# Kernel tuning notes

Measured on AMD Instinct MI355X. Metric: run time of the kernel, lower is better.

Reference implementation:

```python
import jax, jax.numpy as jnp
import numpy as np

B, T, C, H = 2, 2048, 1024, 16
D = C // H  # head dim = 64


def setup_inputs() -> dict:
    key = jax.random.key(0)
    k1, k2, k3 = jax.random.split(key, 3)
    s = 1.0 / np.sqrt(C)
    return {
        "x": jax.random.normal(k1, (B, T, C), dtype=jnp.float32),
        "w_qkv": jax.random.normal(k2, (C, 3 * C), dtype=jnp.float32) * s,
        "b_qkv": jnp.zeros((3 * C,), dtype=jnp.float32),
        "w_proj": jax.random.normal(k3, (C, C), dtype=jnp.float32) * s,
        "b_proj": jnp.zeros((C,), dtype=jnp.float32),
    }


def reference(x, w_qkv, b_qkv, w_proj, b_proj):
    Bx, Tx, Cx = x.shape
    qkv = x @ w_qkv + b_qkv                      # [B,T,3C]
    q, k, v = jnp.split(qkv, 3, axis=-1)         # each [B,T,C]
    # split heads -> [B,H,T,D]
    q = q.reshape(Bx, Tx, H, D).transpose(0, 2, 1, 3)
    k = k.reshape(Bx, Tx, H, D).transpose(0, 2, 1, 3)
    v = v.reshape(Bx, Tx, H, D).transpose(0, 2, 1, 3)
    att = jnp.einsum("bhqd,bhkd->bhqk", q, k) * (1.0 / np.sqrt(D))
    causal = jnp.tril(jnp.ones((Tx, Tx), dtype=bool))
    att = jnp.where(causal, att, -jnp.inf)
    att = jax.nn.softmax(att, axis=-1)
    y = jnp.einsum("bhqk,bhkd->bhqd", att, v)    # [B,H,T,D]
    y = y.transpose(0, 2, 1, 3).reshape(Bx, Tx, Cx)
    return y @ w_proj + b_proj
```

## Files before the change

kernel.cpp:

```cpp
#include <hip/hip_runtime.h>


typedef __attribute__((ext_vector_type(8))) __bf16 bf16x8;
typedef __attribute__((ext_vector_type(4))) __bf16 bf16x4;
typedef __attribute__((ext_vector_type(4))) float f32x4;
typedef __attribute__((ext_vector_type(8))) unsigned short u16x8;
typedef __attribute__((ext_vector_type(4))) unsigned short u16x4;

#define GAS __attribute__((address_space(1)))
#define LAS __attribute__((address_space(3)))

__device__ __forceinline__ unsigned short f2b(float f) {
  unsigned int u = __float_as_uint(f);
  unsigned int r = 0x7FFFu + ((u >> 16) & 1u);
  return (unsigned short)((u + r) >> 16);
}
__device__ __forceinline__ float b2f(unsigned short u) {
  return __uint_as_float((unsigned int)u << 16);
}


__global__ void cvt_f32_to_bf16(const float* __restrict__ src,
                                unsigned short* __restrict__ dst, int n4) {
  int i = blockIdx.x * blockDim.x + threadIdx.x;
  if (i < n4) {
    float4 v = ((const float4*)src)[i];
    u16x4 o = { f2b(v.x), f2b(v.y), f2b(v.z), f2b(v.w) };
    *(u16x4*)(dst + (size_t)i * 4) = o;
  }
}

__global__ void transpose_f32_to_bf16(const float* __restrict__ src,
                                      unsigned short* __restrict__ dst,
                                      int K, int N) {
  __shared__ float tile[32][33];
  int n0 = blockIdx.x * 32, k0 = blockIdx.y * 32;
  int tx = threadIdx.x, ty = threadIdx.y;
#pragma unroll
  for (int i = 0; i < 32; i += 8)
    tile[ty + i][tx] = src[(size_t)(k0 + ty + i) * N + n0 + tx];
  __syncthreads();
#pragma unroll
  for (int i = 0; i < 32; i += 8)
    dst[(size_t)(n0 + ty + i) * K + k0 + tx] = f2b(tile[tx][ty + i]);
}


template <int MODE>
__global__ void __launch_bounds__(256, 3) gemm_bt(
    const unsigned short* __restrict__ A, const unsigned short* __restrict__ Bt,
    const float* __restrict__ bias,
    unsigned short* __restrict__ Oq, unsigned short* __restrict__ Ok,
    unsigned short* __restrict__ Ov, float* __restrict__ Of,
    int M, int N, int K) {
  __shared__ unsigned short smem[3 * 128 * 64];
  unsigned short* As = smem;
  unsigned short* Bs = smem + 3 * 128 * 32;

  const int tid = threadIdx.x;
  const int lane = tid & 63;
  const int wid = tid >> 6;
  const int wr = wid >> 1, wc = wid & 1;
  const int lr = lane & 15, lg = lane >> 4;
  const int m0 = blockIdx.x * 128;
  const int n0 = blockIdx.y * 128;

  f32x4 acc[4][4];
#pragma unroll
  for (int mi = 0; mi < 4; mi++)
#pragma unroll
    for (int ni = 0; ni < 4; ni++) acc[mi][ni] = (f32x4){0.f, 0.f, 0.f, 0.f};

  auto stage = [&](int t, int buf) {
    const int k0 = t * 32;
    unsigned short* Ad = As + buf * (128 * 32);
    unsigned short* Bd = Bs + buf * (128 * 32);
#pragma unroll
    for (int it = 0; it < 2; ++it) {
      const int chunk_u = it * 256 + (tid & ~63);
      const int chunk = chunk_u + lane;
      const int row = chunk >> 2;
      const int col = ((chunk & 3) ^ ((row >> 1) & 3)) * 8;
      __builtin_amdgcn_global_load_lds(
          (GAS unsigned int*)(A + (size_t)(m0 + row) * K + k0 + col),
          (LAS unsigned int*)(Ad + chunk_u * 8), 16, 0, 0);
      __builtin_amdgcn_global_load_lds(
          (GAS unsigned int*)(Bt + (size_t)(n0 + row) * K + k0 + col),
          (LAS unsigned int*)(Bd + chunk_u * 8), 16, 0, 0);
    }
  };

  const int kt = K >> 5;
  const int rsw = (lg ^ ((lr >> 1) & 3)) * 8;

  stage(0, 0);
  stage(1, 1);

  int cur = 0;
  for (int t = 0; t < kt; ++t) {
    __builtin_amdgcn_s_barrier();
    if (t + 2 < kt) {
      int pb = cur + 2; if (pb >= 3) pb -= 3;
      stage(t + 2, pb);
      asm volatile("s_waitcnt vmcnt(8)" ::: "memory");
    } else if (t + 1 < kt) {
      asm volatile("s_waitcnt vmcnt(4)" ::: "memory");
    } else {
      asm volatile("s_waitcnt vmcnt(0)" ::: "memory");
    }
    __builtin_amdgcn_s_barrier();

    const unsigned short* Ab = As + cur * (128 * 32);
    const unsigned short* Bb = Bs + cur * (128 * 32);

    bf16x8 af[4], bfr[4];
#pragma unroll
    for (int mi = 0; mi < 4; mi++)
      af[mi] = *(const bf16x8*)(Ab + (wr * 64 + mi * 16 + lr) * 32 + rsw);
#pragma unroll
    for (int ni = 0; ni < 4; ni++)
      bfr[ni] = *(const bf16x8*)(Bb + (wc * 64 + ni * 16 + lr) * 32 + rsw);
    __builtin_amdgcn_s_setprio(1);
#pragma unroll
    for (int mi = 0; mi < 4; mi++)
#pragma unroll
      for (int ni = 0; ni < 4; ni++)
        acc[mi][ni] = __builtin_amdgcn_mfma_f32_16x16x32_bf16(
            af[mi], bfr[ni], acc[mi][ni], 0, 0, 0);
    __builtin_amdgcn_s_setprio(0);

    cur += 1; if (cur >= 3) cur -= 3;
  }

  const float SCLQ = 0.125f * 1.44269504088896340736f;

  if constexpr (MODE == 1) {
#pragma unroll
    for (int mi = 0; mi < 4; mi++) {
#pragma unroll
      for (int ni = 0; ni < 4; ni++) {
        const int nn = n0 + wc * 64 + ni * 16 + lr;
        const float bv = bias[nn];
#pragma unroll
        for (int r = 0; r < 4; r++) {
          const int mm = m0 + wr * 64 + mi * 16 + lg * 4 + r;
          Of[(size_t)mm * N + nn] = acc[mi][ni][r] + bv;
        }
      }
    }
  } else {
    unsigned short* L = smem;
    const int which = n0 >> 10;
    const float sc = (which == 0) ? SCLQ : 1.0f;
    __syncthreads();
#pragma unroll
    for (int mi = 0; mi < 4; mi++) {
#pragma unroll
      for (int ni = 0; ni < 4; ni++) {
        const int nn_l = wc * 64 + ni * 16 + lr;
        const float bv = bias[n0 + nn_l];
#pragma unroll
        for (int r = 0; r < 4; r++) {
          const int mm_l = wr * 64 + mi * 16 + lg * 4 + r;
          const unsigned short v = f2b((acc[mi][ni][r] + bv) * sc);
          if (which == 2) L[nn_l * 136 + mm_l] = v;
          else            L[mm_l * 136 + nn_l] = v;
        }
      }
    }
    __syncthreads();
    const int b = m0 >> 11;
    const int t0 = m0 & 2047;
    const int h0 = (n0 & 1023) >> 6;
    if (which == 2) {
      const int row = tid >> 1;
      const int hsub = row >> 6, d = row & 63;
      const int tt0 = (tid & 1) * 64;
      const unsigned short* src = L + row * 136 + tt0;
      unsigned short* dst = Ov +
          ((size_t)((b * 16 + h0 + hsub) * 64 + d)) * 2048 + t0 + tt0;
#pragma unroll
      for (int j = 0; j < 8; j++)
        *(u16x8*)(dst + j * 8) = *(const u16x8*)(src + j * 8);
    } else {
      const int mm_l = tid & 127;
      const int hsub = tid >> 7;
      const unsigned short* src = L + mm_l * 136 + hsub * 64;
      unsigned short* base = (which == 0) ? Oq : Ok;
      unsigned short* dst = base +
          ((size_t)(b * 16 + h0 + hsub) * 2048 + t0 + mm_l) * 64;
#pragma unroll
      for (int j = 0; j < 8; j++)
        *(u16x8*)(dst + j * 8) = *(const u16x8*)(src + j * 8);
    }
  }
}


__global__ void __launch_bounds__(256, 3) attn_kernel(
    const unsigned short* __restrict__ Qh, const unsigned short* __restrict__ Kh,
    const unsigned short* __restrict__ Vh, unsigned short* __restrict__ yatt,
    unsigned short* __restrict__ Opart, float* __restrict__ Mp,
    float* __restrict__ Lp) {
  __shared__ unsigned short KsL[2 * 64 * 64];
  __shared__ unsigned short VsL[2 * 64 * 64];
  __shared__ unsigned short Pl[4 * 32 * 72];

  const int tid = threadIdx.x;
  const int lane = tid & 63;
  const int w = tid >> 6;
  const int lr = lane & 15, lg = lane >> 4;

  const int cls = blockIdx.x >> 5;
  const int bh = blockIdx.x & 31;
  const int hh = bh & 15;
  const int bb = bh >> 4;

  const unsigned long long QA = 0x8899AABBCCDDEEFFull;
  const unsigned long long QB = 0x0000014425566377ull;
  const unsigned long long KK = 0x00A4912444444444ull;
  const int qt = (cls < 16) ? (int)((QA >> (4 * cls)) & 15)
                            : (int)((QB >> (4 * (cls - 16))) & 15);
  const int kind = (int)((KK >> (2 * cls)) & 3);
  const int t0 = (kind == 1) ? (qt + 1) : 0;
  const int t1 = (kind == 0) ? (qt + 1) : (2 * qt + 2);

  const size_t head_base = ((size_t)(bb * 16 + hh)) * 2048 * 64;
  const unsigned short* Qg = Qh + head_base;
  const unsigned short* Kg = Kh + head_base;
  const unsigned short* Vg = Vh + head_base;

  const int q0 = qt * 128 + w * 32;
  const int diagw = 2 * qt + (w >> 1);

  bf16x8 aqA0 = *(const bf16x8*)(Qg + (size_t)(q0 + lr) * 64 + lg * 8);
  bf16x8 aqA1 = *(const bf16x8*)(Qg + (size_t)(q0 + lr) * 64 + 32 + lg * 8);
  bf16x8 aqB0 = *(const bf16x8*)(Qg + (size_t)(q0 + 16 + lr) * 64 + lg * 8);
  bf16x8 aqB1 = *(const bf16x8*)(Qg + (size_t)(q0 + 16 + lr) * 64 + 32 + lg * 8);

  float mA = -__builtin_inff(), mB = -__builtin_inff();
  float lA = 0.f, lB = 0.f;
  f32x4 oA[4], oB[4];
#pragma unroll
  for (int dj = 0; dj < 4; dj++) {
    oA[dj] = (f32x4){0.f, 0.f, 0.f, 0.f};
    oB[dj] = (f32x4){0.f, 0.f, 0.f, 0.f};
  }

  auto stage = [&](int kv0, int buf) {
    unsigned short* Kd = KsL + buf * (64 * 64);
    unsigned short* Vd = VsL + buf * (64 * 64);
#pragma unroll
    for (int it = 0; it < 2; ++it) {
      const int chunk_u = it * 256 + (tid & ~63);
      const int chunk = chunk_u + lane;
      const int row = chunk >> 3;
      const int col = ((chunk & 7) ^ (row & 7)) << 3;
      __builtin_amdgcn_global_load_lds(
          (GAS unsigned int*)(Kg + (size_t)(kv0 + row) * 64 + col),
          (LAS unsigned int*)(Kd + chunk_u * 8), 16, 0, 0);
      __builtin_amdgcn_global_load_lds(
          (GAS unsigned int*)(Vg + (size_t)row * 2048 + kv0 + col),
          (LAS unsigned int*)(Vd + chunk_u * 8), 16, 0, 0);
    }
  };

  __bf16* Pw = (__bf16*)(Pl + w * 32 * 72);
  const int swr = (lr & 7) << 3;
  const int pswz = (lr & 3) << 4;

  stage(t0 * 64, t0 & 1);

  for (int i = t0; i < t1; ++i) {
    const int cur = i & 1;
    __builtin_amdgcn_s_barrier();
    if (i + 1 < t1) {
      stage((i + 1) * 64, cur ^ 1);
      asm volatile("s_waitcnt vmcnt(4)" ::: "memory");
    } else {
      asm volatile("s_waitcnt vmcnt(0)" ::: "memory");
    }
    __builtin_amdgcn_s_barrier();

    if (i <= diagw) {
      const int kv0 = i * 64;
      const unsigned short* Kb = KsL + cur * (64 * 64);
      const unsigned short* Vb = VsL + cur * (64 * 64);

      f32x4 sA[4], sB[4];
      __builtin_amdgcn_s_setprio(1);
#pragma unroll
      for (int nj = 0; nj < 4; nj++) {
        const unsigned short* krow = Kb + (nj * 16 + lr) * 64;
        bf16x8 kb0 = *(const bf16x8*)(krow + ((lg * 8) ^ swr));
        bf16x8 kb1 = *(const bf16x8*)(krow + ((32 + lg * 8) ^ swr));
        f32x4 zA = (f32x4){0.f, 0.f, 0.f, 0.f};
        f32x4 zB = (f32x4){0.f, 0.f, 0.f, 0.f};
        zA = __builtin_amdgcn_mfma_f32_16x16x32_bf16(kb0, aqA0, zA, 0, 0, 0);
        zA = __builtin_amdgcn_mfma_f32_16x16x32_bf16(kb1, aqA1, zA, 0, 0, 0);
        zB = __builtin_amdgcn_mfma_f32_16x16x32_bf16(kb0, aqB0, zB, 0, 0, 0);
        zB = __builtin_amdgcn_mfma_f32_16x16x32_bf16(kb1, aqB1, zB, 0, 0, 0);
        sA[nj] = zA;
        sB[nj] = zB;
      }
      __builtin_amdgcn_s_setprio(0);

      if (i == diagw) {
        const int qrA = q0 + lr, qrB = q0 + 16 + lr;
#pragma unroll
        for (int nj = 0; nj < 4; nj++) {
#pragma unroll
          for (int r = 0; r < 4; r++) {
            const int key = kv0 + nj * 16 + lg * 4 + r;
            if (key > qrA) sA[nj][r] = -__builtin_inff();
            if (key > qrB) sB[nj][r] = -__builtin_inff();
          }
        }
      }

      float pmA = sA[0][0], pmB = sB[0][0];
#pragma unroll
      for (int nj = 0; nj < 4; nj++)
#pragma unroll
        for (int r = 0; r < 4; r++) {
          pmA = fmaxf(pmA, sA[nj][r]);
          pmB = fmaxf(pmB, sB[nj][r]);
        }

      const bool okl = (pmA <= mA + 8.f) & (pmB <= mB + 8.f);
      if (!__all(okl)) {
        pmA = fmaxf(pmA, __shfl_xor(pmA, 16));
        pmA = fmaxf(pmA, __shfl_xor(pmA, 32));
        pmB = fmaxf(pmB, __shfl_xor(pmB, 16));
        pmB = fmaxf(pmB, __shfl_xor(pmB, 32));
        const float mnA = fmaxf(mA, pmA), mnB = fmaxf(mB, pmB);
        const float scA = exp2f(mA - mnA), scB = exp2f(mB - mnB);
        mA = mnA; mB = mnB;
        lA *= scA; lB *= scB;
#pragma unroll
        for (int r = 0; r < 4; r++) {
          const float cA = __shfl(scA, lg * 4 + r);
          const float cB = __shfl(scB, lg * 4 + r);
#pragma unroll
          for (int dj = 0; dj < 4; dj++) {
            oA[dj][r] *= cA;
            oB[dj][r] *= cB;
          }
        }
      }

#pragma unroll
      for (int nj = 0; nj < 4; nj++) {
        const float a0 = exp2f(sA[nj][0] - mA), a1 = exp2f(sA[nj][1] - mA);
        const float a2 = exp2f(sA[nj][2] - mA), a3 = exp2f(sA[nj][3] - mA);
        lA += (a0 + a1) + (a2 + a3);
        bf16x4 pkA = {(__bf16)a0, (__bf16)a1, (__bf16)a2, (__bf16)a3};
        *(bf16x4*)(Pw + lr * 72 + ((nj * 16 + lg * 4) ^ pswz)) = pkA;
        const float b0 = exp2f(sB[nj][0] - mB), b1 = exp2f(sB[nj][1] - mB);
        const float b2 = exp2f(sB[nj][2] - mB), b3 = exp2f(sB[nj][3] - mB);
        lB += (b0 + b1) + (b2 + b3);
        bf16x4 pkB = {(__bf16)b0, (__bf16)b1, (__bf16)b2, (__bf16)b3};
        *(bf16x4*)(Pw + (16 + lr) * 72 + ((nj * 16 + lg * 4) ^ pswz)) = pkB;
      }

      bf16x8 paA0 = *(const bf16x8*)(Pw + lr * 72 + ((lg * 8) ^ pswz));
      bf16x8 paA1 = *(const bf16x8*)(Pw + lr * 72 + ((32 + lg * 8) ^ pswz));
      bf16x8 paB0 = *(const bf16x8*)(Pw + (16 + lr) * 72 + ((lg * 8) ^ pswz));
      bf16x8 paB1 = *(const bf16x8*)(Pw + (16 + lr) * 72 + ((32 + lg * 8) ^ pswz));

      __builtin_amdgcn_s_setprio(1);
#pragma unroll
      for (int dj = 0; dj < 4; dj++) {
        const unsigned short* vrow = Vb + (dj * 16 + lr) * 64;
        bf16x8 vb0 = *(const bf16x8*)(vrow + ((lg * 8) ^ swr));
        bf16x8 vb1 = *(const bf16x8*)(vrow + ((32 + lg * 8) ^ swr));
        oA[dj] = __builtin_amdgcn_mfma_f32_16x16x32_bf16(paA0, vb0, oA[dj], 0, 0, 0);
        oA[dj] = __builtin_amdgcn_mfma_f32_16x16x32_bf16(paA1, vb1, oA[dj], 0, 0, 0);
        oB[dj] = __builtin_amdgcn_mfma_f32_16x16x32_bf16(paB0, vb0, oB[dj], 0, 0, 0);
        oB[dj] = __builtin_amdgcn_mfma_f32_16x16x32_bf16(paB1, vb1, oB[dj], 0, 0, 0);
      }
      __builtin_amdgcn_s_setprio(0);
    }
  }

  lA += __shfl_xor(lA, 16); lA += __shfl_xor(lA, 32);
  lB += __shfl_xor(lB, 16); lB += __shfl_xor(lB, 32);

  if (kind == 2) {
    __bf16* yb = (__bf16*)yatt;
#pragma unroll
    for (int r = 0; r < 4; r++) {
      const float invA = 1.0f / __shfl(lA, lg * 4 + r);
      const float invB = 1.0f / __shfl(lB, lg * 4 + r);
      const int tA = q0 + lg * 4 + r;
      const int tB = tA + 16;
      const size_t baseA = ((size_t)(bb * 2048 + tA)) * 1024 + hh * 64;
      const size_t baseB = ((size_t)(bb * 2048 + tB)) * 1024 + hh * 64;
#pragma unroll
      for (int dj = 0; dj < 4; dj++) {
        yb[baseA + dj * 16 + lr] = (__bf16)(oA[dj][r] * invA);
        yb[baseB + dj * 16 + lr] = (__bf16)(oB[dj][r] * invB);
      }
    }
  } else {
    __bf16* Ob = (__bf16*)Opart;
#pragma unroll
    for (int r = 0; r < 4; r++) {
      const int slotA = bh * 1536 + (q0 + lg * 4 + r) - 512;
      const int slotB = slotA + 16;
      const size_t baseA = ((size_t)(kind * 49152 + slotA)) * 64;
      const size_t baseB = ((size_t)(kind * 49152 + slotB)) * 64;
#pragma unroll
      for (int dj = 0; dj < 4; dj++) {
        Ob[baseA + dj * 16 + lr] = (__bf16)oA[dj][r];
        Ob[baseB + dj * 16 + lr] = (__bf16)oB[dj][r];
      }
    }
    if (lg == 0) {
      const int slA = bh * 1536 + (q0 + lr) - 512;
      Mp[kind * 49152 + slA] = mA;
      Lp[kind * 49152 + slA] = lA;
      Mp[kind * 49152 + slA + 16] = mB;
      Lp[kind * 49152 + slA + 16] = lB;
    }
  }
}

__global__ void __launch_bounds__(256) attn_merge(
    const unsigned short* __restrict__ Op, const float* __restrict__ Mp,
    const float* __restrict__ Lp, unsigned short* __restrict__ yatt) {
  const int gid = blockIdx.x * 256 + threadIdx.x;
  const int sl = gid >> 3;
  const int d0 = (gid & 7) * 8;
  const int bh = blockIdx.y;
  const int slot = bh * 1536 + sl;
  const float m1 = Mp[slot], m2 = Mp[49152 + slot];
  const float l1 = Lp[slot], l2 = Lp[49152 + slot];
  const float mx = fmaxf(m1, m2);
  const float w1 = exp2f(m1 - mx), w2 = exp2f(m2 - mx);
  const float inv = 1.0f / (l1 * w1 + l2 * w2);
  u16x8 a = *(const u16x8*)(Op + (size_t)slot * 64 + d0);
  u16x8 b = *(const u16x8*)(Op + (size_t)(49152 + slot) * 64 + d0);
  const int qr = 512 + sl;
  unsigned short* dst = yatt +
      ((size_t)((bh >> 4) * 2048 + qr)) * 1024 + (bh & 15) * 64 + d0;
  u16x8 o;
#pragma unroll
  for (int j = 0; j < 8; j++)
    o[j] = f2b((b2f(a[j]) * w1 + b2f(b[j]) * w2) * inv);
  *(u16x8*)dst = o;
}


extern "C" void kernel_launch(void* const* d_in, const int* in_sizes, int n_in,
                              void* d_out, int out_size, void* d_ws,
                              size_t ws_size, hipStream_t stream) {
  (void)in_sizes; (void)n_in; (void)out_size; (void)ws_size;
  const float* x      = (const float*)d_in[0];
  const float* w_qkv  = (const float*)d_in[1];
  const float* b_qkv  = (const float*)d_in[2];
  const float* w_proj = (const float*)d_in[3];
  const float* b_proj = (const float*)d_in[4];
  float* out = (float*)d_out;

  unsigned short* ws     = (unsigned short*)d_ws;
  unsigned short* xb     = ws;
  unsigned short* wqkvT  = xb     + (size_t)4096 * 1024;
  unsigned short* wprojT = wqkvT  + (size_t)3072 * 1024;
  unsigned short* Qh     = wprojT + (size_t)1024 * 1024;
  unsigned short* Kh     = Qh     + (size_t)2 * 16 * 2048 * 64;
  unsigned short* Vh     = Kh     + (size_t)2 * 16 * 2048 * 64;
  unsigned short* yatt   = Vh     + (size_t)2 * 16 * 2048 * 64;

  unsigned short* Opart = ws;
  float* Mp = (float*)(ws + (size_t)6291456);
  float* Lp = Mp + 2 * 49152;

  cvt_f32_to_bf16<<<4096, 256, 0, stream>>>(x, xb, 1048576);
  transpose_f32_to_bf16<<<dim3(96, 32), dim3(32, 8), 0, stream>>>(w_qkv, wqkvT, 1024, 3072);
  transpose_f32_to_bf16<<<dim3(32, 32), dim3(32, 8), 0, stream>>>(w_proj, wprojT, 1024, 1024);

  gemm_bt<0><<<dim3(32, 24), 256, 0, stream>>>(xb, wqkvT, b_qkv, Qh, Kh, Vh,
                                               nullptr, 4096, 3072, 1024);
  attn_kernel<<<896, 256, 0, stream>>>(Qh, Kh, Vh, yatt, Opart, Mp, Lp);
  attn_merge<<<dim3(48, 32), 256, 0, stream>>>(Opart, Mp, Lp, yatt);
  gemm_bt<1><<<dim3(32, 8), 256, 0, stream>>>(yatt, wprojT, b_proj, nullptr,
                                              nullptr, nullptr, out, 4096, 1024, 1024);
}
```

Measured before the change: 116.0 us.

## Use 256x256 tiles with 512 threads and split-phase pipeline for QKV GEMM

Replaces the templated 128x128 QKV GEMM with a dedicated kernel that uses 256x256 tiles, 8 waves, and a triple-buffered direct global-to-LDS load. Each k-step is split into two halves that interleave prefetch with MFMA work. The epilogue writes the head-split Q/K/V outputs in two passes through LDS. The larger tile raises operand reuse and cuts global traffic, but launches only 192 blocks, which may leave some CUs idle. The projection GEMM keeps the old path as its own kernel.

```diff
diff --git a/kernel.cpp b/kernel.cpp
--- a/kernel.cpp
+++ b/kernel.cpp
@@ -46,13 +46,162 @@
 }
 
 
-template <int MODE>
-__global__ void __launch_bounds__(256, 3) gemm_bt(
+__global__ void __launch_bounds__(512, 2) gemm_qkv256(
     const unsigned short* __restrict__ A, const unsigned short* __restrict__ Bt,
     const float* __restrict__ bias,
     unsigned short* __restrict__ Oq, unsigned short* __restrict__ Ok,
-    unsigned short* __restrict__ Ov, float* __restrict__ Of,
-    int M, int N, int K) {
+    unsigned short* __restrict__ Ov) {
+  constexpr int K = 1024;
+  constexpr int NT = 32;
+  __shared__ unsigned short smem[6 * 256 * 32];
+  unsigned short* As = smem;
+  unsigned short* Bs = smem + 3 * 256 * 32;
+
+  const int tid = threadIdx.x;
+  const int lane = tid & 63;
+  const int wid = tid >> 6;
+  const int wr = wid >> 2;
+  const int wc = wid & 3;
+  const int lr = lane & 15, lg = lane >> 4;
+  const int m0 = blockIdx.x * 256;
+  const int n0 = blockIdx.y * 256;
+
+  f32x4 acc[8][4];
+#pragma unroll
+  for (int mi = 0; mi < 8; mi++)
+#pragma unroll
+    for (int ni = 0; ni < 4; ni++) acc[mi][ni] = (f32x4){0.f, 0.f, 0.f, 0.f};
+
+  auto stageHalf = [&](int t, int buf, int mh) {
+    const int k0 = t * 32;
+    unsigned short* Ad = As + buf * (256 * 32);
+    unsigned short* Bd = Bs + buf * (256 * 32);
+    const int chunk = mh * 512 + tid;
+    const int chunk_u = mh * 512 + (tid & ~63);
+    const int row = chunk >> 2;
+    const int col = ((chunk & 3) ^ ((row >> 1) & 3)) * 8;
+    __builtin_amdgcn_global_load_lds(
+        (GAS unsigned int*)(A + (size_t)(m0 + row) * K + k0 + col),
+        (LAS unsigned int*)(Ad + chunk_u * 8), 16, 0, 0);
+    __builtin_amdgcn_global_load_lds(
+        (GAS unsigned int*)(Bt + (size_t)(n0 + row) * K + k0 + col),
+        (LAS unsigned int*)(Bd + chunk_u * 8), 16, 0, 0);
+  };
+
+  const int rsw = (lg ^ ((lr >> 1) & 3)) * 8;
+
+  stageHalf(0, 0, 0); stageHalf(0, 0, 1);
+  stageHalf(1, 1, 0); stageHalf(1, 1, 1);
+  asm volatile("s_waitcnt vmcnt(4)" ::: "memory");
+  __builtin_amdgcn_s_barrier();
+
+  int bj = 0;
+  for (int j = 0; j < NT; ++j) {
+    const unsigned short* Ab = As + bj * (256 * 32);
+    const unsigned short* Bb = Bs + bj * (256 * 32);
+    int bp = bj + 2; if (bp >= 3) bp -= 3;
+    const bool pf = (j + 2 < NT);
+
+    bf16x8 bfr[4], af[4];
+#pragma unroll
+    for (int ni = 0; ni < 4; ni++)
+      bfr[ni] = *(const bf16x8*)(Bb + (wc * 64 + ni * 16 + lr) * 32 + rsw);
+#pragma unroll
+    for (int mi = 0; mi < 4; mi++)
+      af[mi] = *(const bf16x8*)(Ab + (wr * 128 + mi * 16 + lr) * 32 + rsw);
+    if (pf) stageHalf(j + 2, bp, 0);
+    __builtin_amdgcn_s_barrier();
+    asm volatile("s_waitcnt lgkmcnt(0)" ::: "memory");
+    __builtin_amdgcn_sched_barrier(0);
+    __builtin_amdgcn_s_setprio(1);
+#pragma unroll
+    for (int mi = 0; mi < 4; mi++)
+#pragma unroll
+      for (int ni = 0; ni < 4; ni++)
+        acc[mi][ni] = __builtin_amdgcn_mfma_f32_16x16x32_bf16(
+            af[mi], bfr[ni], acc[mi][ni], 0, 0, 0);
+    __builtin_amdgcn_s_setprio(0);
+    __builtin_amdgcn_s_barrier();
+
+#pragma unroll
+    for (int mi = 0; mi < 4; mi++)
+      af[mi] = *(const bf16x8*)(Ab + (wr * 128 + (4 + mi) * 16 + lr) * 32 + rsw);
+    if (pf) stageHalf(j + 2, bp, 1);
+    __builtin_amdgcn_s_barrier();
+    asm volatile("s_waitcnt lgkmcnt(0)" ::: "memory");
+    __builtin_amdgcn_sched_barrier(0);
+    __builtin_amdgcn_s_setprio(1);
+#pragma unroll
+    for (int mi = 0; mi < 4; mi++)
+#pragma unroll
+      for (int ni = 0; ni < 4; ni++)
+        acc[4 + mi][ni] = __builtin_amdgcn_mfma_f32_16x16x32_bf16(
+            af[mi], bfr[ni], acc[4 + mi][ni], 0, 0, 0);
+    __builtin_amdgcn_s_setprio(0);
+    if (pf) asm volatile("s_waitcnt vmcnt(4)" ::: "memory");
+    else    asm volatile("s_waitcnt vmcnt(0)" ::: "memory");
+    __builtin_amdgcn_s_barrier();
+
+    bj += 1; if (bj >= 3) bj -= 3;
+  }
+
+  const float SCLQ = 0.125f * 1.44269504088896340736f;
+  const int which = n0 >> 10;
+  const int h0 = (n0 & 1023) >> 6;
+  const float sc = (which == 0) ? SCLQ : 1.0f;
+  unsigned short* L = smem;
+
+#pragma unroll
+  for (int h = 0; h < 2; ++h) {
+    __syncthreads();
+    if (wr == h) {
+#pragma unroll
+      for (int mi = 0; mi < 8; mi++) {
+#pragma unroll
+        for (int ni = 0; ni < 4; ni++) {
+          const int col_l = wc * 64 + ni * 16 + lr;
+          const float bv = bias[n0 + col_l];
+#pragma unroll
+          for (int r = 0; r < 4; r++) {
+            const int row_l = mi * 16 + lg * 4 + r;
+            const unsigned short v = f2b((acc[mi][ni][r] + bv) * sc);
+            if (which == 2) L[col_l * 136 + row_l] = v;
+            else            L[row_l * 264 + col_l] = v;
+          }
+        }
+      }
+    }
+    __syncthreads();
+    const int b = (m0 + h * 128) >> 11;
+    if (which == 2) {
+      const int nn_l = tid >> 1, half = tid & 1;
+      const int d = nn_l & 63, head = h0 + (nn_l >> 6);
+      const unsigned short* src = L + nn_l * 136 + half * 64;
+      unsigned short* dst = Ov +
+          ((size_t)((b * 16 + head) * 64 + d)) * 2048 +
+          ((m0 + h * 128 + half * 64) & 2047);
+#pragma unroll
+      for (int jj = 0; jj < 8; jj++)
+        *(u16x8*)(dst + jj * 8) = *(const u16x8*)(src + jj * 8);
+    } else {
+      const int mm_l = tid >> 2, seg = tid & 3;
+      const int tt = (m0 + h * 128 + mm_l) & 2047;
+      const unsigned short* src = L + mm_l * 264 + seg * 64;
+      unsigned short* base = (which == 0) ? Oq : Ok;
+      unsigned short* dst = base +
+          ((size_t)((b * 16 + h0 + seg) * 2048 + tt)) * 64;
+#pragma unroll
+      for (int jj = 0; jj < 8; jj++)
+        *(u16x8*)(dst + jj * 8) = *(const u16x8*)(src + jj * 8);
+    }
+  }
+}
+
+
+__global__ void __launch_bounds__(256, 3) gemm_proj(
+    const unsigned short* __restrict__ A, const unsigned short* __restrict__ Bt,
+    const float* __restrict__ bias, float* __restrict__ Of, int M, int N,
+    int K) {
   __shared__ unsigned short smem[3 * 128 * 64];
   unsigned short* As = smem;
   unsigned short* Bs = smem + 3 * 128 * 32;
@@ -132,66 +281,17 @@
     cur += 1; if (cur >= 3) cur -= 3;
   }
 
-  const float SCLQ = 0.125f * 1.44269504088896340736f;
-
-  if constexpr (MODE == 1) {
-#pragma unroll
-    for (int mi = 0; mi < 4; mi++) {
-#pragma unroll
-      for (int ni = 0; ni < 4; ni++) {
-        const int nn = n0 + wc * 64 + ni * 16 + lr;
-        const float bv = bias[nn];
-#pragma unroll
-        for (int r = 0; r < 4; r++) {
-          const int mm = m0 + wr * 64 + mi * 16 + lg * 4 + r;
-          Of[(size_t)mm * N + nn] = acc[mi][ni][r] + bv;
-        }
-      }
-    }
-  } else {
-    unsigned short* L = smem;
-    const int which = n0 >> 10;
-    const float sc = (which == 0) ? SCLQ : 1.0f;
-    __syncthreads();
-#pragma unroll
-    for (int mi = 0; mi < 4; mi++) {
-#pragma unroll
-      for (int ni = 0; ni < 4; ni++) {
-        const int nn_l = wc * 64 + ni * 16 + lr;
-        const float bv = bias[n0 + nn_l];
-#pragma unroll
-        for (int r = 0; r < 4; r++) {
-          const int mm_l = wr * 64 + mi * 16 + lg * 4 + r;
-          const unsigned short v = f2b((acc[mi][ni][r] + bv) * sc);
-          if (which == 2) L[nn_l * 136 + mm_l] = v;
-          else            L[mm_l * 136 + nn_l] = v;
-        }
-      }
-    }
-    __syncthreads();
-    const int b = m0 >> 11;
-    const int t0 = m0 & 2047;
-    const int h0 = (n0 & 1023) >> 6;
-    if (which == 2) {
-      const int row = tid >> 1;
-      const int hsub = row >> 6, d = row & 63;
-      const int tt0 = (tid & 1) * 64;
-      const unsigned short* src = L + row * 136 + tt0;
-      unsigned short* dst = Ov +
-          ((size_t)((b * 16 + h0 + hsub) * 64 + d)) * 2048 + t0 + tt0;
-#pragma unroll
-      for (int j = 0; j < 8; j++)
-        *(u16x8*)(dst + j * 8) = *(const u16x8*)(src + j * 8);
-    } else {
-      const int mm_l = tid & 127;
-      const int hsub = tid >> 7;
-      const unsigned short* src = L + mm_l * 136 + hsub * 64;
-      unsigned short* base = (which == 0) ? Oq : Ok;
-      unsigned short* dst = base +
-          ((size_t)(b * 16 + h0 + hsub) * 2048 + t0 + mm_l) * 64;
-#pragma unroll
-      for (int j = 0; j < 8; j++)
-        *(u16x8*)(dst + j * 8) = *(const u16x8*)(src + j * 8);
+#pragma unroll
+  for (int mi = 0; mi < 4; mi++) {
+#pragma unroll
+    for (int ni = 0; ni < 4; ni++) {
+      const int nn = n0 + wc * 64 + ni * 16 + lr;
+      const float bv = bias[nn];
+#pragma unroll
+      for (int r = 0; r < 4; r++) {
+        const int mm = m0 + wr * 64 + mi * 16 + lg * 4 + r;
+        Of[(size_t)mm * N + nn] = acc[mi][ni][r] + bv;
+      }
     }
   }
 }
@@ -480,10 +580,9 @@
   transpose_f32_to_bf16<<<dim3(96, 32), dim3(32, 8), 0, stream>>>(w_qkv, wqkvT, 1024, 3072);
   transpose_f32_to_bf16<<<dim3(32, 32), dim3(32, 8), 0, stream>>>(w_proj, wprojT, 1024, 1024);
 
-  gemm_bt<0><<<dim3(32, 24), 256, 0, stream>>>(xb, wqkvT, b_qkv, Qh, Kh, Vh,
-                                               nullptr, 4096, 3072, 1024);
+  gemm_qkv256<<<dim3(16, 12), 512, 0, stream>>>(xb, wqkvT, b_qkv, Qh, Kh, Vh);
   attn_kernel<<<896, 256, 0, stream>>>(Qh, Kh, Vh, yatt, Opart, Mp, Lp);
   attn_merge<<<dim3(48, 32), 256, 0, stream>>>(Opart, Mp, Lp, yatt);
-  gemm_bt<1><<<dim3(32, 8), 256, 0, stream>>>(yatt, wprojT, b_proj, nullptr,
-                                              nullptr, nullptr, out, 4096, 1024, 1024);
-}
+  gemm_proj<<<dim3(32, 8), 256, 0, stream>>>(yatt, wprojT, b_proj, out,
+                                             4096, 1024, 1024);
+}
```

Result: slower. 123.7 us (+6.6%).
